# Kernel optimization log

Measured on AMD Instinct MI355X. Metric: run time of the kernel, lower is better.

The kernel has to match this reference:

```python
import jax, jax.numpy as jnp
import numpy as np

D_MODEL = 256
N_HEADS = 8
D_FF = 1024
N_LAYERS = 6
INPUT_DIM = 2
EPS = 1e-5  # torch LayerNorm default


def _layer_norm(x, g, b):
    m = jnp.mean(x, axis=-1, keepdims=True)
    v = jnp.mean((x - m) ** 2, axis=-1, keepdims=True)
    return (x - m) / jnp.sqrt(v + EPS) * g + b


def setup_inputs() -> dict:
    key = jax.random.key(0)
    ks = jax.random.split(key, 8)
    f32 = jnp.float32

    def w(k, shape, fan_in):
        return jax.random.normal(k, shape, f32) * (1.0 / np.sqrt(fan_in))

    return {
        "x": jax.random.normal(ks[0], (8, 1024, INPUT_DIM), f32),
        "in_w": w(ks[1], (INPUT_DIM, D_MODEL), INPUT_DIM),
        "in_b": jnp.zeros((D_MODEL,), f32),
        "ln1_g": jnp.ones((D_MODEL,), f32),
        "ln1_b": jnp.zeros((D_MODEL,), f32),
        "qkv_w": w(ks[2], (D_MODEL, 3 * D_MODEL), D_MODEL),
        "qkv_b": jnp.zeros((3 * D_MODEL,), f32),
        "out_w": w(ks[3], (D_MODEL, D_MODEL), D_MODEL),
        "out_b": jnp.zeros((D_MODEL,), f32),
        "lna_g": jnp.ones((D_MODEL,), f32),
        "lna_b": jnp.zeros((D_MODEL,), f32),
        "ln2_g": jnp.ones((D_MODEL,), f32),
        "ln2_b": jnp.zeros((D_MODEL,), f32),
        "ff1_w": w(ks[4], (D_MODEL, D_FF), D_MODEL),
        "ff1_b": jnp.zeros((D_FF,), f32),
        "ff2_w": w(ks[5], (D_FF, D_MODEL), D_FF),
        "ff2_b": jnp.zeros((D_MODEL,), f32),
        "lnf_g": jnp.ones((D_MODEL,), f32),
        "lnf_b": jnp.zeros((D_MODEL,), f32),
    }


def reference(x, in_w, in_b, ln1_g, ln1_b, qkv_w, qkv_b, out_w, out_b,
              lna_g, lna_b, ln2_g, ln2_b, ff1_w, ff1_b, ff2_w, ff2_b,
              lnf_g, lnf_b):
    B, L, _ = x.shape
    dk = D_MODEL // N_HEADS
    scale = 1.0 / np.sqrt(dk)
    top_k = max(1, L // 4)

    # sinusoidal positional encoding [L, D]
    pos = jnp.arange(L, dtype=jnp.float32)[:, None]
    div = jnp.exp(jnp.arange(0, D_MODEL, 2, dtype=jnp.float32)
                  * (-np.log(10000.0) / D_MODEL))
    pe = jnp.zeros((L, D_MODEL), jnp.float32)
    pe = pe.at[:, 0::2].set(jnp.sin(pos * div))
    pe = pe.at[:, 1::2].set(jnp.cos(pos * div))

    h = x @ in_w + in_b + pe[None]  # [B, L, D]

    # VoformerEncoder reuses the SAME layer object -> shared weights, 6 passes
    for _ in range(N_LAYERS):
        # --- self-attention sublayer (pre-norm) ---
        s2 = _layer_norm(h, ln1_g, ln1_b)
        qkv = (s2 @ qkv_w + qkv_b).reshape(B, L, 3, N_HEADS, dk)
        q = qkv[:, :, 0].transpose(0, 2, 1, 3)  # [B, H, L, dk]
        k = qkv[:, :, 1].transpose(0, 2, 1, 3)
        v = qkv[:, :, 2].transpose(0, 2, 1, 3)

        scores = jnp.einsum('bhqd,bhkd->bhqk', q, k) * scale  # [B,H,L,L]
        # ProbSparse: keep only the per-row top-k scores
        thr = jax.lax.top_k(scores, top_k)[0][..., -1:]
        sparse = jnp.where(scores >= thr, scores, -jnp.inf)
        attn = jax.nn.softmax(sparse, axis=-1)
        o = jnp.einsum('bhqk,bhkd->bhqd', attn, v)
        o = o.transpose(0, 2, 1, 3).reshape(B, L, D_MODEL)
        o = o @ out_w + out_b
        # InformerAttention applies its own residual + LayerNorm
        attn_out = _layer_norm(o + s2, lna_g, lna_b)
        h = h + attn_out

        # --- FFN sublayer with Volatilite activation ---
        s2 = _layer_norm(h, ln2_g, ln2_b)
        f = s2 @ ff1_w + ff1_b  # [B, L, d_ff]
        mean_f = jnp.mean(f, axis=1, keepdims=True)
        vol = jnp.sqrt(jnp.mean((mean_f - f) ** 2, axis=1, keepdims=True))
        f = f * vol
        f = f @ ff2_w + ff2_b
        h = h + f

    return _layer_norm(h, lnf_g, lnf_b)
```

## Files before the change

### kernel.cpp

```cpp
#include <hip/hip_runtime.h>
#include <math.h>

#define D_MODEL 256
#define NH 8
#define DFF 1024
#define NLAYERS 6
#define B_ 8
#define L_ 1024
#define NR (B_*L_)
#define TOPK 256
#define LNEPS 1e-5f

typedef __attribute__((ext_vector_type(8))) short bf16x8;
typedef __attribute__((ext_vector_type(4))) float f32x4;

__device__ __forceinline__ float wsum(float v){
  #pragma unroll
  for(int o=32;o>0;o>>=1) v += __shfl_xor(v,o,64);
  return v;
}
__device__ __forceinline__ short f2bf(float x){
  unsigned u = __float_as_uint(x);
  u += 0x7fffu + ((u>>16)&1u);
  return (short)(u>>16);
}
__device__ __forceinline__ float bf2f(short s){
  return __uint_as_float(((unsigned)(unsigned short)s)<<16);
}
__device__ __forceinline__ int sortkey(unsigned u){
  return (u & 0x8000u) ? (int)(u ^ 0xFFFFu) : (int)(u | 0x8000u);
}
__device__ __forceinline__ float kinvf(int k){
  unsigned u = (k & 0x8000) ? ((unsigned)k ^ 0x8000u) : ((unsigned)k ^ 0xFFFFu);
  return __uint_as_float(u << 16);
}
__device__ __forceinline__ void g2l(const short* g, short* l){
  __builtin_amdgcn_global_load_lds(
      (const __attribute__((address_space(1))) unsigned int*)g,
      (__attribute__((address_space(3))) unsigned int*)l,
      16, 0, 0);
}

__global__ __launch_bounds__(256) void embed_kernel(
    const float* __restrict__ x, const float* __restrict__ in_w,
    const float* __restrict__ in_b, float* __restrict__ h)
{
  int tid = blockIdx.x*256 + threadIdx.x;
  int n  = tid >> 6;
  int d0 = (tid & 63) << 2;
  int l  = n & (L_-1);
  float x0 = x[2*n], x1 = x[2*n+1];
  const float kf = -0.07195578415606394f;
  float pe[4];
  #pragma unroll
  for(int ii=0; ii<2; ++ii){
    int i = (d0>>1) + ii;
    float dv  = expf((float)i * kf);
    float ang = (float)l * dv;
    pe[2*ii]   = sinf(ang);
    pe[2*ii+1] = cosf(ang);
  }
  float4 w0 = *(const float4*)(in_w + d0);
  float4 w1 = *(const float4*)(in_w + D_MODEL + d0);
  float4 bb = *(const float4*)(in_b + d0);
  float4 o;
  o.x = x0*w0.x + x1*w1.x + bb.x + pe[0];
  o.y = x0*w0.y + x1*w1.y + bb.y + pe[1];
  o.z = x0*w0.z + x1*w1.z + bb.z + pe[2];
  o.w = x0*w0.w + x1*w1.w + bb.w + pe[3];
  *(float4*)(h + (size_t)n*D_MODEL + d0) = o;
}

__global__ __launch_bounds__(256) void wcvt(
    const float* __restrict__ W, short* __restrict__ WT, int N, int kshift)
{
  int idx = blockIdx.x*256 + threadIdx.x;
  int K = 1<<kshift;
  if (idx >= N*K) return;
  int n = idx >> kshift, k = idx & (K-1);
  WT[idx] = f2bf(W[(size_t)k*N + n]);
}

template<int OM>
__global__ __launch_bounds__(256) void ln_kernel(
    const float* __restrict__ in, const float* __restrict__ g,
    const float* __restrict__ b, float* __restrict__ out,
    short* __restrict__ outb)
{
  int wave = threadIdx.x >> 6, lane = threadIdx.x & 63;
  int row = blockIdx.x*4 + wave;
  float4 v = ((const float4*)(in + (size_t)row*D_MODEL))[lane];
  float s  = v.x+v.y+v.z+v.w;
  float sq = v.x*v.x+v.y*v.y+v.z*v.z+v.w*v.w;
  s = wsum(s); sq = wsum(sq);
  float mean = s*(1.f/D_MODEL);
  float var  = sq*(1.f/D_MODEL) - mean*mean;
  float rstd = 1.f/sqrtf(var + LNEPS);
  float4 gv = ((const float4*)g)[lane];
  float4 bv = ((const float4*)b)[lane];
  float4 o;
  o.x = (v.x-mean)*rstd*gv.x + bv.x;
  o.y = (v.y-mean)*rstd*gv.y + bv.y;
  o.z = (v.z-mean)*rstd*gv.z + bv.z;
  o.w = (v.w-mean)*rstd*gv.w + bv.w;
  if (OM == 0){
    ((float4*)(out + (size_t)row*D_MODEL))[lane] = o;
  }
  if (OM == 2){
    short4 s4; s4.x=f2bf(o.x); s4.y=f2bf(o.y); s4.z=f2bf(o.z); s4.w=f2bf(o.w);
    *(short4*)(outb + (size_t)row*D_MODEL + lane*4) = s4;
  }
}

__global__ __launch_bounds__(256) void lnln_kernel(
    const float* __restrict__ tb,
    const float* __restrict__ ga, const float* __restrict__ ba,
    const float* __restrict__ g2, const float* __restrict__ b2,
    float* __restrict__ h, short* __restrict__ s2b)
{
  int wave = threadIdx.x >> 6, lane = threadIdx.x & 63;
  int row = blockIdx.x*4 + wave;
  float4 v = ((const float4*)(tb + (size_t)row*D_MODEL))[lane];
  float s  = v.x+v.y+v.z+v.w;
  float sq = v.x*v.x+v.y*v.y+v.z*v.z+v.w*v.w;
  s = wsum(s); sq = wsum(sq);
  float mean = s*(1.f/D_MODEL);
  float var  = sq*(1.f/D_MODEL) - mean*mean;
  float rstd = 1.f/sqrtf(var + LNEPS);
  float4 gv = ((const float4*)ga)[lane];
  float4 bv = ((const float4*)ba)[lane];
  float4* hp = (float4*)(h + (size_t)row*D_MODEL) + lane;
  float4 hv = *hp;
  float4 hn;
  hn.x = hv.x + (v.x-mean)*rstd*gv.x + bv.x;
  hn.y = hv.y + (v.y-mean)*rstd*gv.y + bv.y;
  hn.z = hv.z + (v.z-mean)*rstd*gv.z + bv.z;
  hn.w = hv.w + (v.w-mean)*rstd*gv.w + bv.w;
  *hp = hn;
  float s2  = hn.x+hn.y+hn.z+hn.w;
  float sq2 = hn.x*hn.x+hn.y*hn.y+hn.z*hn.z+hn.w*hn.w;
  s2 = wsum(s2); sq2 = wsum(sq2);
  float m2 = s2*(1.f/D_MODEL);
  float v2 = sq2*(1.f/D_MODEL) - m2*m2;
  float r2 = 1.f/sqrtf(v2 + LNEPS);
  float4 g2v = ((const float4*)g2)[lane];
  float4 b2v = ((const float4*)b2)[lane];
  short4 s4;
  s4.x = f2bf((hn.x-m2)*r2*g2v.x + b2v.x);
  s4.y = f2bf((hn.y-m2)*r2*g2v.y + b2v.y);
  s4.z = f2bf((hn.z-m2)*r2*g2v.z + b2v.z);
  s4.w = f2bf((hn.w-m2)*r2*g2v.w + b2v.w);
  *(short4*)(s2b + (size_t)row*D_MODEL + lane*4) = s4;
}

template<int MODE>
__global__ __launch_bounds__(256) void mfma_gemm(
    const short* __restrict__ A, const short* __restrict__ BT,
    const float* __restrict__ bias, const short* __restrict__ residb,
    float* __restrict__ Cf, short* __restrict__ Cb, short* __restrict__ Vt,
    int N, int K)
{
  __shared__ __align__(16) short As[128*32];
  __shared__ __align__(16) short Bs[64*32];
  const int t = threadIdx.x, wv = t>>6, lane = t&63;
  const int r16 = lane&15, quad = lane>>4;
  const int m0 = blockIdx.y*128, n0 = blockIdx.x*64;
  const int ia0 = wv*128 + lane, ia1 = ia0 + 64;
  const int ib  = wv*64 + lane;
  const short* Ab = A  + (size_t)m0*K;
  const short* Bb = BT + (size_t)n0*K;
  const f32x4 z = {0.f,0.f,0.f,0.f};
  f32x4 acc[2][4];
  #pragma unroll
  for (int i=0;i<2;++i)
    #pragma unroll
    for (int j=0;j<4;++j) acc[i][j] = z;

  for (int k0 = 0; k0 < K; k0 += 32){
    __syncthreads();
    g2l(Ab + (size_t)(ia0>>2)*K + k0 + (ia0&3)*8, As + ia0*8);
    g2l(Ab + (size_t)(ia1>>2)*K + k0 + (ia1&3)*8, As + ia1*8);
    g2l(Bb + (size_t)(ib>>2)*K  + k0 + (ib&3)*8,  Bs + ib*8);
    __syncthreads();
    bf16x8 af0 = *(const bf16x8*)(As + ((wv*32      + r16)*32 + quad*8));
    bf16x8 af1 = *(const bf16x8*)(As + ((wv*32 + 16 + r16)*32 + quad*8));
    bf16x8 bf[4];
    #pragma unroll
    for (int ct=0; ct<4; ++ct)
      bf[ct] = *(const bf16x8*)(Bs + ((ct*16 + r16)*32 + quad*8));
    #pragma unroll
    for (int ct=0; ct<4; ++ct){
      acc[0][ct] = __builtin_amdgcn_mfma_f32_16x16x32_bf16(af0, bf[ct], acc[0][ct], 0,0,0);
      acc[1][ct] = __builtin_amdgcn_mfma_f32_16x16x32_bf16(af1, bf[ct], acc[1][ct], 0,0,0);
    }
  }

  #pragma unroll
  for (int rt=0; rt<2; ++rt){
    const int mb = m0 + wv*32 + rt*16 + quad*4;
    #pragma unroll
    for (int ct=0; ct<4; ++ct){
      const int n = n0 + ct*16 + r16;
      const float bv = bias[n];
      if (MODE == 0){
        if (n < 512){
          int region = n>>8, hh = (n>>5)&7, d = n&31;
          #pragma unroll
          for (int r=0;r<4;++r){
            int l = mb + r;
            size_t base = (((size_t)(region*64 + (l>>10)*8 + hh))*1024 + (l&1023))*32 + d;
            Cb[base] = f2bf(acc[rt][ct][r] + bv);
          }
        } else {
          int dv = n - 512, hh = dv>>5, d = dv&31;
          int b = mb>>10, lloc = mb&1023;
          size_t base = (((size_t)(b*8 + hh))*32 + d)*1024 + lloc;
          short4 s4;
          s4.x = f2bf(acc[rt][ct][0] + bv); s4.y = f2bf(acc[rt][ct][1] + bv);
          s4.z = f2bf(acc[rt][ct][2] + bv); s4.w = f2bf(acc[rt][ct][3] + bv);
          *(short4*)(Vt + base) = s4;
        }
      } else {
        #pragma unroll
        for (int r=0;r<4;++r){
          size_t off = (size_t)(mb + r)*N + n;
          float c = acc[rt][ct][r] + bv;
          if (MODE == 1) Cf[off] = c + bf2f(residb[off]);
          if (MODE == 2) Cb[off] = f2bf(c);
          if (MODE == 3) Cf[off] += c;
        }
      }
    }
  }
}

__global__ __launch_bounds__(256,4) void attn_mfma(
    const short* __restrict__ qkbf, const short* __restrict__ vT,
    short* __restrict__ ob)
{
  __shared__ __align__(16) short sc16[16*1024];
  __shared__ float linv[16];
  const int t = threadIdx.x, wv = t>>6, lane = t&63;
  const int r16 = lane&15, quad = lane>>4;
  const int blk = blockIdx.x;
  const int bh = (blk & 7)*8 + ((blk>>3)&7);
  const int qt = blk >> 6;

  bf16x8 aq = *(const bf16x8*)(qkbf + ((size_t)bh*1024 + qt*16 + r16)*32 + quad*8);
  const short* kb = qkbf + (size_t)(64 + bh)*1024*32;

  bf16x8 bk[16];
  #pragma unroll
  for (int tt=0; tt<16; ++tt)
    bk[tt] = *(const bf16x8*)(kb + (size_t)(wv*256 + tt*16 + r16)*32 + quad*8);
  #pragma unroll
  for (int tt=0; tt<16; ++tt){
    f32x4 c = {0.f,0.f,0.f,0.f};
    c = __builtin_amdgcn_mfma_f32_16x16x32_bf16(aq, bk[tt], c, 0, 0, 0);
    const int pos = wv*256 + ((tt ^ quad)<<4) + r16;
    #pragma unroll
    for (int r=0;r<4;++r)
      sc16[(quad*4+r)*1024 + pos] = f2bf(c[r]);
  }
  __syncthreads();

  const float SC2 = 0.25500529485087056f;
  const int sw = wv << 4;
  short* prow = sc16 + ((2*lane) ^ sw);
  for (int rp=0; rp<2; ++rp){
    const int ra = wv*4 + rp*2;
    short* pa = prow + ra*1024;
    short* pb = pa + 1024;
    unsigned wa[8], wb[8];
    #pragma unroll
    for (int i=0;i<8;++i){
      wa[i] = *(const unsigned*)(pa + i*128);
      wb[i] = *(const unsigned*)(pb + i*128);
    }
    int ka[16], kb2[16];
    #pragma unroll
    for (int i=0;i<8;++i){
      ka[2*i]    = sortkey(wa[i] & 0xFFFFu);
      ka[2*i+1]  = sortkey(wa[i] >> 16);
      kb2[2*i]   = sortkey(wb[i] & 0xFFFFu);
      kb2[2*i+1] = sortkey(wb[i] >> 16);
    }
    int mxa = ka[0], mxb = kb2[0];
    #pragma unroll
    for (int i=1;i<16;++i){
      mxa = (ka[i]  > mxa) ? ka[i]  : mxa;
      mxb = (kb2[i] > mxb) ? kb2[i] : mxb;
    }
    #pragma unroll
    for (int o=32;o>0;o>>=1){
      int sa = __shfl_xor(mxa, o, 64); mxa = (sa > mxa) ? sa : mxa;
      int sb = __shfl_xor(mxb, o, 64); mxb = (sb > mxb) ? sb : mxb;
    }
    int loA=0, hiA=mxa+1, loB=0, hiB=mxb+1;
    while (hiA-loA > 1 || hiB-loB > 1){
      int midA = (loA+hiA)>>1, midB = (loB+hiB)>>1;
      int cA=0, cB=0;
      #pragma unroll
      for (int i=0;i<16;++i){
        cA += (int)__popcll(__ballot(ka[i]  >= midA));
        cB += (int)__popcll(__ballot(kb2[i] >= midB));
      }
      if (cA >= TOPK) loA = midA; else hiA = midA;
      if (cB >= TOPK) loB = midB; else hiB = midB;
    }
    const float thrA = kinvf(loA), thrB = kinvf(loB);
    const float nmA = -kinvf(mxa)*SC2, nmB = -kinvf(mxb)*SC2;
    float suma = 0.f, sumb = 0.f;
    unsigned pka[8], pkb[8];
    #pragma unroll
    for (int i=0;i<8;++i){
      float a0 = __uint_as_float(wa[i] << 16);
      float a1 = __uint_as_float(wa[i] & 0xFFFF0000u);
      float b0 = __uint_as_float(wb[i] << 16);
      float b1 = __uint_as_float(wb[i] & 0xFFFF0000u);
      float ea0 = (a0 >= thrA) ? exp2f(fmaf(a0, SC2, nmA)) : 0.f;
      float ea1 = (a1 >= thrA) ? exp2f(fmaf(a1, SC2, nmA)) : 0.f;
      float eb0 = (b0 >= thrB) ? exp2f(fmaf(b0, SC2, nmB)) : 0.f;
      float eb1 = (b1 >= thrB) ? exp2f(fmaf(b1, SC2, nmB)) : 0.f;
      suma += ea0 + ea1; sumb += eb0 + eb1;
      pka[i] = (unsigned)(unsigned short)f2bf(ea0) | ((unsigned)(unsigned short)f2bf(ea1) << 16);
      pkb[i] = (unsigned)(unsigned short)f2bf(eb0) | ((unsigned)(unsigned short)f2bf(eb1) << 16);
    }
    suma = wsum(suma); sumb = wsum(sumb);
    if (lane == 0){ linv[ra] = 1.f/suma; linv[ra+1] = 1.f/sumb; }
    #pragma unroll
    for (int i=0;i<8;++i){
      *(unsigned*)(pa + i*128) = pka[i];
      *(unsigned*)(pb + i*128) = pkb[i];
    }
  }
  __syncthreads();

  const short* vb = vT + (size_t)bh*32*1024;
  bf16x8 bvv[16];
  #pragma unroll
  for (int tt=0; tt<8; ++tt){
    int k0 = wv*256 + tt*32;
    #pragma unroll
    for (int n=0;n<2;++n)
      bvv[tt*2+n] = *(const bf16x8*)(vb + (size_t)(n*16 + r16)*1024 + k0 + quad*8);
  }
  const int sA = ((r16>>2)&3) << 4;
  f32x4 oa0 = {0.f,0.f,0.f,0.f}, oa1 = {0.f,0.f,0.f,0.f};
  #pragma unroll
  for (int tt=0; tt<8; ++tt){
    int k0 = wv*256 + tt*32;
    bf16x8 af = *(const bf16x8*)(sc16 + r16*1024 + ((k0 + quad*8) ^ sA));
    oa0 = __builtin_amdgcn_mfma_f32_16x16x32_bf16(af, bvv[tt*2+0], oa0, 0, 0, 0);
    oa1 = __builtin_amdgcn_mfma_f32_16x16x32_bf16(af, bvv[tt*2+1], oa1, 0, 0, 0);
  }
  __syncthreads();
  float* po = (float*)sc16;
  #pragma unroll
  for (int r=0;r<4;++r){
    po[wv*512 + (quad*4+r)*32 +      r16] = oa0[r];
    po[wv*512 + (quad*4+r)*32 + 16 + r16] = oa1[r];
  }
  __syncthreads();
  int e = t*2;
  float v0 = po[e]   + po[512+e]   + po[1024+e]   + po[1536+e];
  float v1 = po[e+1] + po[512+e+1] + po[1024+e+1] + po[1536+e+1];
  int q = e>>5, d = e&31;
  const float inv = linv[q];
  int b = bh>>3, hh = bh&7;
  size_t off = ((size_t)(b*1024 + qt*16 + q))*256 + hh*32 + d;
  short2 s2o; s2o.x = f2bf(v0*inv); s2o.y = f2bf(v1*inv);
  *(short2*)(ob + off) = s2o;
}

__global__ __launch_bounds__(512) void vol_scale(short* __restrict__ f)
{
  __shared__ float ps[8][64], pq[8][64], vs[64];
  int b = blockIdx.x >> 4, cb = blockIdx.x & 15;
  int cl = threadIdx.x & 63, sl = threadIdx.x >> 6;
  int col = cb*64 + cl;
  short* fb = f + (size_t)b*L_*DFF + col;
  float s = 0.f, sq = 0.f;
  for (int l = sl*128; l < sl*128+128; ++l){
    float v = bf2f(fb[(size_t)l*DFF]);
    s += v; sq += v*v;
  }
  ps[sl][cl] = s; pq[sl][cl] = sq;
  __syncthreads();
  if (threadIdx.x < 64){
    float st=0.f, qt=0.f;
    #pragma unroll
    for (int i=0;i<8;++i){ st += ps[i][cl]; qt += pq[i][cl]; }
    float mean = st*(1.f/L_);
    float var  = qt*(1.f/L_) - mean*mean;
    vs[cl] = sqrtf(fmaxf(var, 0.f));
  }
  __syncthreads();
  float vv = vs[cl];
  for (int l = sl*128; l < sl*128+128; ++l){
    size_t o = (size_t)l*DFF;
    fb[o] = f2bf(bf2f(fb[o]) * vv);
  }
}

extern "C" void kernel_launch(void* const* d_in, const int* in_sizes, int n_in,
                              void* d_out, int out_size, void* d_ws, size_t ws_size,
                              hipStream_t stream) {
  const float* x     = (const float*)d_in[0];
  const float* in_w  = (const float*)d_in[1];
  const float* in_b  = (const float*)d_in[2];
  const float* ln1_g = (const float*)d_in[3];
  const float* ln1_b = (const float*)d_in[4];
  const float* qkv_w = (const float*)d_in[5];
  const float* qkv_b = (const float*)d_in[6];
  const float* out_w = (const float*)d_in[7];
  const float* out_b = (const float*)d_in[8];
  const float* lna_g = (const float*)d_in[9];
  const float* lna_b = (const float*)d_in[10];
  const float* ln2_g = (const float*)d_in[11];
  const float* ln2_b = (const float*)d_in[12];
  const float* ff1_w = (const float*)d_in[13];
  const float* ff1_b = (const float*)d_in[14];
  const float* ff2_w = (const float*)d_in[15];
  const float* ff2_b = (const float*)d_in[16];
  const float* lnf_g = (const float*)d_in[17];
  const float* lnf_b = (const float*)d_in[18];
  float* out = (float*)d_out;

  char* ws = (char*)d_ws;
  float* h     = (float*)(ws);
  short* s2b   = (short*)(ws + (size_t)( 8<<20));
  short* qkbf  = (short*)(ws + (size_t)(12<<20));
  short* vTb   = (short*)(ws + (size_t)(20<<20));
  short* ob_b  = (short*)(ws + (size_t)(24<<20));
  short* f     = (short*)(ws + (size_t)(12<<20));
  float* tb    = (float*)(ws + (size_t)(28<<20));
  short* qkvwT = (short*)(ws + (size_t)(36<<20));
  short* outwT = (short*)(ws + (size_t)(36<<20) + 393216);
  short* ff1wT = (short*)(ws + (size_t)(36<<20) + 393216 + 131072);
  short* ff2wT = (short*)(ws + (size_t)(36<<20) + 393216 + 131072 + 524288);

  embed_kernel<<<NR*64/256, 256, 0, stream>>>(x, in_w, in_b, h);
  wcvt<<< 768, 256, 0, stream>>>(qkv_w, qkvwT,  768, 8);
  wcvt<<< 256, 256, 0, stream>>>(out_w, outwT,  256, 8);
  wcvt<<<1024, 256, 0, stream>>>(ff1_w, ff1wT, 1024, 8);
  wcvt<<<1024, 256, 0, stream>>>(ff2_w, ff2wT,  256, 10);

  for (int layer = 0; layer < NLAYERS; ++layer){
    ln_kernel<2><<<NR/4, 256, 0, stream>>>(h, ln1_g, ln1_b, nullptr, s2b);
    {
      dim3 g(768/64, NR/128);
      mfma_gemm<0><<<g, 256, 0, stream>>>(s2b, qkvwT, qkv_b, nullptr,
                                          nullptr, qkbf, vTb, 768, 256);
    }
    attn_mfma<<<64*64, 256, 0, stream>>>(qkbf, vTb, ob_b);
    {
      dim3 g(256/64, NR/128);
      mfma_gemm<1><<<g, 256, 0, stream>>>(ob_b, outwT, out_b, s2b,
                                          tb, nullptr, nullptr, 256, 256);
    }
    lnln_kernel<<<NR/4, 256, 0, stream>>>(tb, lna_g, lna_b, ln2_g, ln2_b, h, s2b);
    {
      dim3 g(1024/64, NR/128);
      mfma_gemm<2><<<g, 256, 0, stream>>>(s2b, ff1wT, ff1_b, nullptr,
                                          nullptr, f, nullptr, 1024, 256);
    }
    vol_scale<<<B_*16, 512, 0, stream>>>(f);
    {
      dim3 g(256/64, NR/128);
      mfma_gemm<3><<<g, 256, 0, stream>>>(f, ff2wT, ff2_b, nullptr,
                                          h, nullptr, nullptr, 256, 1024);
    }
  }
  ln_kernel<0><<<NR/4, 256, 0, stream>>>(h, lnf_g, lnf_b, out, nullptr);
}
```

Measured before the change: 1.282 ms.

## Widen GEMM N-tile, fixed-bit top-k search, new LDS swizzle, packed bf16 stores

The GEMM is templated on M-tile size and now covers 128 output columns per block with 8 MFMA column tiles per wave, so A-tile reuse goes up and fewer blocks are launched. The attention kernel switches its top-k threshold search from a data-dependent binary search to a fixed 16-bit radix descent. It also changes the LDS swizzle for the score tile and folds the softmax normalisation into the probabilities before the PV MFMA, instead of scaling the output afterwards. Packed bf16 conversion via the hip_bf16 intrinsic replaces the manual per-element rounding. The larger tiles raise register pressure and reduce grid parallelism for the N=256 GEMMs, and normalising before the bf16 cast slightly changes rounding.

```diff
diff --git a/kernel.cpp b/kernel.cpp
--- a/kernel.cpp
+++ b/kernel.cpp
@@ -1,4 +1,5 @@
 #include <hip/hip_runtime.h>
+#include <hip/hip_bf16.h>
 #include <math.h>
 
 #define D_MODEL 256
@@ -26,6 +27,11 @@
 }
 __device__ __forceinline__ float bf2f(short s){
   return __uint_as_float(((unsigned)(unsigned short)s)<<16);
+}
+__device__ __forceinline__ unsigned pk2bf(float a, float b){
+  __hip_bfloat162 h = __float22bfloat162_rn(make_float2(a,b));
+  unsigned u; __builtin_memcpy(&u, &h, 4);
+  return u;
 }
 __device__ __forceinline__ int sortkey(unsigned u){
   return (u & 0x8000u) ? (int)(u ^ 0xFFFFu) : (int)(u | 0x8000u);
@@ -107,8 +113,8 @@
     ((float4*)(out + (size_t)row*D_MODEL))[lane] = o;
   }
   if (OM == 2){
-    short4 s4; s4.x=f2bf(o.x); s4.y=f2bf(o.y); s4.z=f2bf(o.z); s4.w=f2bf(o.w);
-    *(short4*)(outb + (size_t)row*D_MODEL + lane*4) = s4;
+    uint2 pk; pk.x = pk2bf(o.x, o.y); pk.y = pk2bf(o.z, o.w);
+    *(uint2*)(outb + (size_t)row*D_MODEL + lane*4) = pk;
   }
 }
 
@@ -145,61 +151,67 @@
   float r2 = 1.f/sqrtf(v2 + LNEPS);
   float4 g2v = ((const float4*)g2)[lane];
   float4 b2v = ((const float4*)b2)[lane];
-  short4 s4;
-  s4.x = f2bf((hn.x-m2)*r2*g2v.x + b2v.x);
-  s4.y = f2bf((hn.y-m2)*r2*g2v.y + b2v.y);
-  s4.z = f2bf((hn.z-m2)*r2*g2v.z + b2v.z);
-  s4.w = f2bf((hn.w-m2)*r2*g2v.w + b2v.w);
-  *(short4*)(s2b + (size_t)row*D_MODEL + lane*4) = s4;
-}
-
-template<int MODE>
+  uint2 pk;
+  pk.x = pk2bf((hn.x-m2)*r2*g2v.x + b2v.x, (hn.y-m2)*r2*g2v.y + b2v.y);
+  pk.y = pk2bf((hn.z-m2)*r2*g2v.z + b2v.z, (hn.w-m2)*r2*g2v.w + b2v.w);
+  *(uint2*)(s2b + (size_t)row*D_MODEL + lane*4) = pk;
+}
+
+template<int MODE, int TM>
 __global__ __launch_bounds__(256) void mfma_gemm(
     const short* __restrict__ A, const short* __restrict__ BT,
     const float* __restrict__ bias, const short* __restrict__ residb,
     float* __restrict__ Cf, short* __restrict__ Cb, short* __restrict__ Vt,
     int N, int K)
 {
-  __shared__ __align__(16) short As[128*32];
-  __shared__ __align__(16) short Bs[64*32];
+  constexpr int MT = TM/64;
+  __shared__ __align__(16) short As[TM*32];
+  __shared__ __align__(16) short Bs[128*32];
   const int t = threadIdx.x, wv = t>>6, lane = t&63;
   const int r16 = lane&15, quad = lane>>4;
-  const int m0 = blockIdx.y*128, n0 = blockIdx.x*64;
-  const int ia0 = wv*128 + lane, ia1 = ia0 + 64;
-  const int ib  = wv*64 + lane;
+  const int m0 = blockIdx.y*TM, n0 = blockIdx.x*128;
   const short* Ab = A  + (size_t)m0*K;
   const short* Bb = BT + (size_t)n0*K;
   const f32x4 z = {0.f,0.f,0.f,0.f};
-  f32x4 acc[2][4];
-  #pragma unroll
-  for (int i=0;i<2;++i)
-    #pragma unroll
-    for (int j=0;j<4;++j) acc[i][j] = z;
+  f32x4 acc[MT][8];
+  #pragma unroll
+  for (int i=0;i<MT;++i)
+    #pragma unroll
+    for (int j=0;j<8;++j) acc[i][j] = z;
 
   for (int k0 = 0; k0 < K; k0 += 32){
     __syncthreads();
-    g2l(Ab + (size_t)(ia0>>2)*K + k0 + (ia0&3)*8, As + ia0*8);
-    g2l(Ab + (size_t)(ia1>>2)*K + k0 + (ia1&3)*8, As + ia1*8);
-    g2l(Bb + (size_t)(ib>>2)*K  + k0 + (ib&3)*8,  Bs + ib*8);
+    #pragma unroll
+    for (int j=0;j<MT;++j){
+      int c = j*256 + wv*64 + lane;
+      g2l(Ab + (size_t)(c>>2)*K + k0 + (c&3)*8, As + c*8);
+    }
+    #pragma unroll
+    for (int j=0;j<2;++j){
+      int c = j*256 + wv*64 + lane;
+      g2l(Bb + (size_t)(c>>2)*K + k0 + (c&3)*8, Bs + c*8);
+    }
     __syncthreads();
-    bf16x8 af0 = *(const bf16x8*)(As + ((wv*32      + r16)*32 + quad*8));
-    bf16x8 af1 = *(const bf16x8*)(As + ((wv*32 + 16 + r16)*32 + quad*8));
-    bf16x8 bf[4];
-    #pragma unroll
-    for (int ct=0; ct<4; ++ct)
+    bf16x8 af[MT];
+    #pragma unroll
+    for (int mt=0;mt<MT;++mt)
+      af[mt] = *(const bf16x8*)(As + ((wv*MT*16 + mt*16 + r16)*32 + quad*8));
+    bf16x8 bf[8];
+    #pragma unroll
+    for (int ct=0;ct<8;++ct)
       bf[ct] = *(const bf16x8*)(Bs + ((ct*16 + r16)*32 + quad*8));
     #pragma unroll
-    for (int ct=0; ct<4; ++ct){
-      acc[0][ct] = __builtin_amdgcn_mfma_f32_16x16x32_bf16(af0, bf[ct], acc[0][ct], 0,0,0);
-      acc[1][ct] = __builtin_amdgcn_mfma_f32_16x16x32_bf16(af1, bf[ct], acc[1][ct], 0,0,0);
-    }
-  }
-
-  #pragma unroll
-  for (int rt=0; rt<2; ++rt){
-    const int mb = m0 + wv*32 + rt*16 + quad*4;
-    #pragma unroll
-    for (int ct=0; ct<4; ++ct){
+    for (int ct=0;ct<8;++ct)
+      #pragma unroll
+      for (int mt=0;mt<MT;++mt)
+        acc[mt][ct] = __builtin_amdgcn_mfma_f32_16x16x32_bf16(af[mt], bf[ct], acc[mt][ct], 0,0,0);
+  }
+
+  #pragma unroll
+  for (int mt=0;mt<MT;++mt){
+    const int mb = m0 + wv*MT*16 + mt*16 + quad*4;
+    #pragma unroll
+    for (int ct=0;ct<8;++ct){
       const int n = n0 + ct*16 + r16;
       const float bv = bias[n];
       if (MODE == 0){
@@ -209,22 +221,22 @@
           for (int r=0;r<4;++r){
             int l = mb + r;
             size_t base = (((size_t)(region*64 + (l>>10)*8 + hh))*1024 + (l&1023))*32 + d;
-            Cb[base] = f2bf(acc[rt][ct][r] + bv);
+            Cb[base] = f2bf(acc[mt][ct][r] + bv);
           }
         } else {
           int dv = n - 512, hh = dv>>5, d = dv&31;
           int b = mb>>10, lloc = mb&1023;
           size_t base = (((size_t)(b*8 + hh))*32 + d)*1024 + lloc;
-          short4 s4;
-          s4.x = f2bf(acc[rt][ct][0] + bv); s4.y = f2bf(acc[rt][ct][1] + bv);
-          s4.z = f2bf(acc[rt][ct][2] + bv); s4.w = f2bf(acc[rt][ct][3] + bv);
-          *(short4*)(Vt + base) = s4;
+          uint2 pk;
+          pk.x = pk2bf(acc[mt][ct][0] + bv, acc[mt][ct][1] + bv);
+          pk.y = pk2bf(acc[mt][ct][2] + bv, acc[mt][ct][3] + bv);
+          *(uint2*)(Vt + base) = pk;
         }
       } else {
         #pragma unroll
         for (int r=0;r<4;++r){
           size_t off = (size_t)(mb + r)*N + n;
-          float c = acc[rt][ct][r] + bv;
+          float c = acc[mt][ct][r] + bv;
           if (MODE == 1) Cf[off] = c + bf2f(residb[off]);
           if (MODE == 2) Cb[off] = f2bf(c);
           if (MODE == 3) Cf[off] += c;
@@ -239,7 +251,6 @@
     short* __restrict__ ob)
 {
   __shared__ __align__(16) short sc16[16*1024];
-  __shared__ float linv[16];
   const int t = threadIdx.x, wv = t>>6, lane = t&63;
   const int r16 = lane&15, quad = lane>>4;
   const int blk = blockIdx.x;
@@ -253,85 +264,89 @@
   #pragma unroll
   for (int tt=0; tt<16; ++tt)
     bk[tt] = *(const bf16x8*)(kb + (size_t)(wv*256 + tt*16 + r16)*32 + quad*8);
+  short* p0 = sc16 + quad*4096;
   #pragma unroll
   for (int tt=0; tt<16; ++tt){
     f32x4 c = {0.f,0.f,0.f,0.f};
     c = __builtin_amdgcn_mfma_f32_16x16x32_bf16(aq, bk[tt], c, 0, 0, 0);
-    const int pos = wv*256 + ((tt ^ quad)<<4) + r16;
-    #pragma unroll
-    for (int r=0;r<4;++r)
-      sc16[(quad*4+r)*1024 + pos] = f2bf(c[r]);
+    const int keyq = (wv*256 + tt*16 + r16) ^ ((quad&1)<<5);
+    unsigned u01 = pk2bf(c[0], c[1]);
+    unsigned u23 = pk2bf(c[2], c[3]);
+    p0[keyq]               = (short)u01;
+    p0[1024 + (keyq ^ 8)]  = (short)(u01>>16);
+    p0[2048 + (keyq ^ 16)] = (short)u23;
+    p0[3072 + (keyq ^ 24)] = (short)(u23>>16);
   }
   __syncthreads();
 
   const float SC2 = 0.25500529485087056f;
-  const int sw = wv << 4;
-  short* prow = sc16 + ((2*lane) ^ sw);
+  #pragma unroll
   for (int rp=0; rp<2; ++rp){
     const int ra = wv*4 + rp*2;
-    short* pa = prow + ra*1024;
-    short* pb = pa + 1024;
+    const int sa = (ra&7)<<3;
+    short* pa = sc16 + ra*1024 + ((2*lane) ^ sa);
+    short* pb = sc16 + (ra+1)*1024 + (((2*lane) ^ sa) ^ 8);
     unsigned wa[8], wb[8];
     #pragma unroll
     for (int i=0;i<8;++i){
       wa[i] = *(const unsigned*)(pa + i*128);
       wb[i] = *(const unsigned*)(pb + i*128);
     }
-    int ka[16], kb2[16];
+    int ka[16], kbk[16];
     #pragma unroll
     for (int i=0;i<8;++i){
       ka[2*i]    = sortkey(wa[i] & 0xFFFFu);
       ka[2*i+1]  = sortkey(wa[i] >> 16);
-      kb2[2*i]   = sortkey(wb[i] & 0xFFFFu);
-      kb2[2*i+1] = sortkey(wb[i] >> 16);
-    }
-    int mxa = ka[0], mxb = kb2[0];
+      kbk[2*i]   = sortkey(wb[i] & 0xFFFFu);
+      kbk[2*i+1] = sortkey(wb[i] >> 16);
+    }
+    int mxa = ka[0], mxb = kbk[0];
     #pragma unroll
     for (int i=1;i<16;++i){
       mxa = (ka[i]  > mxa) ? ka[i]  : mxa;
-      mxb = (kb2[i] > mxb) ? kb2[i] : mxb;
+      mxb = (kbk[i] > mxb) ? kbk[i] : mxb;
     }
     #pragma unroll
     for (int o=32;o>0;o>>=1){
-      int sa = __shfl_xor(mxa, o, 64); mxa = (sa > mxa) ? sa : mxa;
-      int sb = __shfl_xor(mxb, o, 64); mxb = (sb > mxb) ? sb : mxb;
-    }
-    int loA=0, hiA=mxa+1, loB=0, hiB=mxb+1;
-    while (hiA-loA > 1 || hiB-loB > 1){
-      int midA = (loA+hiA)>>1, midB = (loB+hiB)>>1;
-      int cA=0, cB=0;
+      int sA = __shfl_xor(mxa, o, 64); mxa = (sA > mxa) ? sA : mxa;
+      int sB = __shfl_xor(mxb, o, 64); mxb = (sB > mxb) ? sB : mxb;
+    }
+    int loA = 0, loB = 0;
+    #pragma unroll
+    for (int bit = 15; bit >= 0; --bit){
+      const int midA = loA + (1<<bit);
+      const int midB = loB + (1<<bit);
+      int cA = 0, cB = 0;
       #pragma unroll
       for (int i=0;i<16;++i){
         cA += (int)__popcll(__ballot(ka[i]  >= midA));
-        cB += (int)__popcll(__ballot(kb2[i] >= midB));
+        cB += (int)__popcll(__ballot(kbk[i] >= midB));
       }
-      if (cA >= TOPK) loA = midA; else hiA = midA;
-      if (cB >= TOPK) loB = midB; else hiB = midB;
+      if (cA >= TOPK) loA = midA;
+      if (cB >= TOPK) loB = midB;
     }
     const float thrA = kinvf(loA), thrB = kinvf(loB);
     const float nmA = -kinvf(mxa)*SC2, nmB = -kinvf(mxb)*SC2;
+    float ea0[8], ea1[8], eb0[8], eb1[8];
     float suma = 0.f, sumb = 0.f;
-    unsigned pka[8], pkb[8];
     #pragma unroll
     for (int i=0;i<8;++i){
       float a0 = __uint_as_float(wa[i] << 16);
       float a1 = __uint_as_float(wa[i] & 0xFFFF0000u);
       float b0 = __uint_as_float(wb[i] << 16);
       float b1 = __uint_as_float(wb[i] & 0xFFFF0000u);
-      float ea0 = (a0 >= thrA) ? exp2f(fmaf(a0, SC2, nmA)) : 0.f;
-      float ea1 = (a1 >= thrA) ? exp2f(fmaf(a1, SC2, nmA)) : 0.f;
-      float eb0 = (b0 >= thrB) ? exp2f(fmaf(b0, SC2, nmB)) : 0.f;
-      float eb1 = (b1 >= thrB) ? exp2f(fmaf(b1, SC2, nmB)) : 0.f;
-      suma += ea0 + ea1; sumb += eb0 + eb1;
-      pka[i] = (unsigned)(unsigned short)f2bf(ea0) | ((unsigned)(unsigned short)f2bf(ea1) << 16);
-      pkb[i] = (unsigned)(unsigned short)f2bf(eb0) | ((unsigned)(unsigned short)f2bf(eb1) << 16);
+      ea0[i] = (a0 >= thrA) ? exp2f(fmaf(a0, SC2, nmA)) : 0.f;
+      ea1[i] = (a1 >= thrA) ? exp2f(fmaf(a1, SC2, nmA)) : 0.f;
+      eb0[i] = (b0 >= thrB) ? exp2f(fmaf(b0, SC2, nmB)) : 0.f;
+      eb1[i] = (b1 >= thrB) ? exp2f(fmaf(b1, SC2, nmB)) : 0.f;
+      suma += ea0[i] + ea1[i]; sumb += eb0[i] + eb1[i];
     }
     suma = wsum(suma); sumb = wsum(sumb);
-    if (lane == 0){ linv[ra] = 1.f/suma; linv[ra+1] = 1.f/sumb; }
+    const float inva = 1.f/suma, invb = 1.f/sumb;
     #pragma unroll
     for (int i=0;i<8;++i){
-      *(unsigned*)(pa + i*128) = pka[i];
-      *(unsigned*)(pb + i*128) = pkb[i];
+      *(unsigned*)(pa + i*128) = pk2bf(ea0[i]*inva, ea1[i]*inva);
+      *(unsigned*)(pb + i*128) = pk2bf(eb0[i]*invb, eb1[i]*invb);
     }
   }
   __syncthreads();
@@ -345,7 +360,7 @@
     for (int n=0;n<2;++n)
       bvv[tt*2+n] = *(const bf16x8*)(vb + (size_t)(n*16 + r16)*1024 + k0 + quad*8);
   }
-  const int sA = ((r16>>2)&3) << 4;
+  const int sA = (r16&7) << 3;
   f32x4 oa0 = {0.f,0.f,0.f,0.f}, oa1 = {0.f,0.f,0.f,0.f};
   #pragma unroll
   for (int tt=0; tt<8; ++tt){
@@ -366,11 +381,9 @@
   float v0 = po[e]   + po[512+e]   + po[1024+e]   + po[1536+e];
   float v1 = po[e+1] + po[512+e+1] + po[1024+e+1] + po[1536+e+1];
   int q = e>>5, d = e&31;
-  const float inv = linv[q];
   int b = bh>>3, hh = bh&7;
   size_t off = ((size_t)(b*1024 + qt*16 + q))*256 + hh*32 + d;
-  short2 s2o; s2o.x = f2bf(v0*inv); s2o.y = f2bf(v1*inv);
-  *(short2*)(ob + off) = s2o;
+  *(unsigned*)(ob + off) = pk2bf(v0, v1);
 }
 
 __global__ __launch_bounds__(512) void vol_scale(short* __restrict__ f)
@@ -449,27 +462,27 @@
   for (int layer = 0; layer < NLAYERS; ++layer){
     ln_kernel<2><<<NR/4, 256, 0, stream>>>(h, ln1_g, ln1_b, nullptr, s2b);
     {
-      dim3 g(768/64, NR/128);
-      mfma_gemm<0><<<g, 256, 0, stream>>>(s2b, qkvwT, qkv_b, nullptr,
-                                          nullptr, qkbf, vTb, 768, 256);
+      dim3 g(768/128, NR/128);
+      mfma_gemm<0,128><<<g, 256, 0, stream>>>(s2b, qkvwT, qkv_b, nullptr,
+                                              nullptr, qkbf, vTb, 768, 256);
     }
     attn_mfma<<<64*64, 256, 0, stream>>>(qkbf, vTb, ob_b);
     {
-      dim3 g(256/64, NR/128);
-      mfma_gemm<1><<<g, 256, 0, stream>>>(ob_b, outwT, out_b, s2b,
-                                          tb, nullptr, nullptr, 256, 256);
+      dim3 g(256/128, NR/64);
+      mfma_gemm<1,64><<<g, 256, 0, stream>>>(ob_b, outwT, out_b, s2b,
+                                             tb, nullptr, nullptr, 256, 256);
     }
     lnln_kernel<<<NR/4, 256, 0, stream>>>(tb, lna_g, lna_b, ln2_g, ln2_b, h, s2b);
     {
-      dim3 g(1024/64, NR/128);
-      mfma_gemm<2><<<g, 256, 0, stream>>>(s2b, ff1wT, ff1_b, nullptr,
-                                          nullptr, f, nullptr, 1024, 256);
+      dim3 g(1024/128, NR/128);
+      mfma_gemm<2,128><<<g, 256, 0, stream>>>(s2b, ff1wT, ff1_b, nullptr,
+                                              nullptr, f, nullptr, 1024, 256);
     }
     vol_scale<<<B_*16, 512, 0, stream>>>(f);
     {
-      dim3 g(256/64, NR/128);
-      mfma_gemm<3><<<g, 256, 0, stream>>>(f, ff2wT, ff2_b, nullptr,
-                                          h, nullptr, nullptr, 256, 1024);
+      dim3 g(256/128, NR/64);
+      mfma_gemm<3,64><<<g, 256, 0, stream>>>(f, ff2wT, ff2_b, nullptr,
+                                             h, nullptr, nullptr, 256, 1024);
     }
   }
   ln_kernel<0><<<NR/4, 256, 0, stream>>>(h, lnf_g, lnf_b, out, nullptr);
```

After: 1.281 ms. Within noise of the previous version (-0.1%).
